# Kernel optimization log

Measured on AMD Instinct MI355X. Metric: run time of the kernel, lower is better.

## Reference

```python
import jax, jax.numpy as jnp
import numpy as np
import math

H = 12  # num_heads
LOGIT_SCALE_MAX = math.log(1.0 / 0.01)  # ~4.60517


def setup_inputs() -> dict:
    key = jax.random.key(0)
    ks = jax.random.split(key, 4)
    L, N, C = 1024, 8, 768
    scale = (C // H) ** -0.5
    return {
        "x": jax.random.normal(ks[0], (L, N, C), jnp.float32),
        "in_proj_weight": jax.random.normal(ks[1], (3 * C, C), jnp.float32) * scale,
        "in_proj_bias": jnp.zeros((3 * C,), jnp.float32),
        "logit_scale": jnp.full((H, 1, 1), jnp.log(10.0), jnp.float32),
        "head_scale": jnp.ones((H, 1, 1), jnp.float32),
        "out_w": jax.random.normal(ks[2], (C, C), jnp.float32) * scale,
        "out_b": jnp.zeros((C,), jnp.float32),
    }


def _normalize(t, eps=1e-12):
    # torch F.normalize: x / max(||x||, eps)
    n = jnp.linalg.norm(t, axis=-1, keepdims=True)
    return t / jnp.maximum(n, eps)


def reference(x, in_proj_weight, in_proj_bias, logit_scale, head_scale, out_w, out_b):
    L, N, C = x.shape
    D = C // H
    qkv = x @ in_proj_weight.T + in_proj_bias  # (L, N, 3C)
    q, k, v = jnp.split(qkv, 3, axis=-1)

    def to_heads(t):  # (L, N, C) -> (N, H, L, D); matches view(L, N*H, D).transpose(0,1)
        return t.reshape(L, N, H, D).transpose(1, 2, 0, 3)

    q, k, v = to_heads(q), to_heads(k), to_heads(v)
    # scaled-cosine attention: cosine sim * clamped-exp learnable logit scale
    attn = jnp.einsum('nhld,nhmd->nhlm', _normalize(q), _normalize(k))  # (N,H,L,L)
    ls = jnp.exp(jnp.minimum(logit_scale, LOGIT_SCALE_MAX))  # (H,1,1)
    attn = attn * ls[None]
    attn = jax.nn.softmax(attn, axis=-1)
    o = jnp.einsum('nhlm,nhmd->nhld', attn, v)  # (N,H,L,D)
    o = o * head_scale[None]  # per-head scale
    o = o.transpose(2, 0, 1, 3).reshape(L, N, C)  # back to (L, N, C)
    return o @ out_w.T + out_b
```

## Files before the change

kernel.cpp:

```cpp
#include <hip/hip_runtime.h>
#include <stdint.h>
#include <math.h>

typedef unsigned short u16;
typedef _Float16 f16;
typedef __attribute__((ext_vector_type(4))) float f32x4;
typedef __attribute__((ext_vector_type(8))) f16 h8;
typedef __attribute__((ext_vector_type(4))) f16 h4;
typedef __attribute__((ext_vector_type(2))) f16 h2;
typedef __attribute__((ext_vector_type(2))) __fp16 fp16x2;
typedef __attribute__((ext_vector_type(4))) unsigned int u32x4;
typedef __attribute__((ext_vector_type(4))) unsigned short u16x4;
typedef __attribute__((ext_vector_type(8))) unsigned short u16x8;

typedef const __attribute__((address_space(1))) u16 gas_u16;
typedef __attribute__((address_space(3))) u16 las_u16;

#define MFMA32(a,b,c) __builtin_amdgcn_mfma_f32_16x16x32_f16((a),(b),(c),0,0,0)
#define MFMA16(a,b,c) __builtin_amdgcn_mfma_f32_16x16x16f16((a),(b),(c),0,0,0)

__device__ __forceinline__ float h2f(u16 h){ f16 x; __builtin_memcpy(&x,&h,2); return (float)x; }
__device__ __forceinline__ u16 f2h(float f){ f16 x = (f16)f; u16 u; __builtin_memcpy(&u,&x,2); return u; }

__device__ __forceinline__ float fast_exp2(float x){
#if __has_builtin(__builtin_amdgcn_exp2f)
  return __builtin_amdgcn_exp2f(x);
#else
  return exp2f(x);
#endif
}

__device__ __forceinline__ h2 pkrtz(float a, float b){
  fp16x2 t = __builtin_amdgcn_cvt_pkrtz(a, b);
  h2 r; __builtin_memcpy(&r, &t, 4);
  return r;
}

#define NA4 1572864
#define NB4 442368
#define NC4 147456
__global__ __launch_bounds__(256) void cvt3_kernel(
    const float* __restrict__ a, u16* __restrict__ da,
    const float* __restrict__ b, u16* __restrict__ db,
    const float* __restrict__ c, u16* __restrict__ dc)
{
  int i = blockIdx.x*256 + threadIdx.x;
  const float* s; u16* d; int off;
  if (i < NA4)            { s = a; d = da; off = i; }
  else if (i < NA4+NB4)   { s = b; d = db; off = i - NA4; }
  else if (i < NA4+NB4+NC4){ s = c; d = dc; off = i - NA4 - NB4; }
  else return;
  f32x4 v = ((const f32x4*)s)[off];
  u16x4 o;
  o[0]=f2h(v[0]); o[1]=f2h(v[1]); o[2]=f2h(v[2]); o[3]=f2h(v[3]);
  ((u16x4*)d)[off] = o;
}

__global__ __launch_bounds__(256) void gemm_kernel(
    const u16* __restrict__ A, const u16* __restrict__ B, const float* __restrict__ bias,
    int mode, u16* __restrict__ qh, u16* __restrict__ kh, u16* __restrict__ vh,
    float* __restrict__ outp, const float* __restrict__ lsb)
{
  __shared__ u16 lA[2][128*64];
  __shared__ u16 lB[2][128*64];
  const int tid = threadIdx.x;
  const int lane = tid & 63;
  const int w = tid >> 6, wr = w >> 1, wc = w & 1;
  const int lo = lane & 15, hi = lane >> 4;

  const int bx = blockIdx.x, by = blockIdx.y;

  f32x4 zero = {0.f,0.f,0.f,0.f};
  f32x4 acc[4][4];
#pragma unroll
  for (int a=0;a<4;a++)
#pragma unroll
    for (int b=0;b<4;b++) acc[a][b] = zero;
  const u16* Ag = A + (size_t)bx*128*768;
  const u16* Bg = B + (size_t)by*128*768;
  const int srow = tid >> 3;
  const int scol = (((tid & 7) ^ (srow & 7)) * 8);

#define STAGE(buf, kt) do { \
    _Pragma("unroll") \
    for (int j=0;j<4;j++) { \
      __builtin_amdgcn_global_load_lds((gas_u16*)(Ag + (size_t)(j*32+srow)*768 + (kt) + scol), (las_u16*)(&lA[buf][j*2048 + tid*8]), 16, 0, 0); \
      __builtin_amdgcn_global_load_lds((gas_u16*)(Bg + (size_t)(j*32+srow)*768 + (kt) + scol), (las_u16*)(&lB[buf][j*2048 + tid*8]), 16, 0, 0); \
    } \
  } while(0)

  STAGE(0, 0);
#pragma unroll
  for (int t = 0; t < 12; ++t) {
    const int cur = t & 1;
    if (t < 11) {
      STAGE(cur^1, (t+1)*64);
      asm volatile("s_waitcnt vmcnt(8)" ::: "memory");
    } else {
      asm volatile("s_waitcnt vmcnt(0)" ::: "memory");
    }
    __builtin_amdgcn_sched_barrier(0);
    __builtin_amdgcn_s_barrier();
#pragma unroll
    for (int kk=0;kk<2;kk++) {
      h8 af[4], bfr[4];
#pragma unroll
      for (int mf=0; mf<4; mf++) {
        int r = wr*64 + mf*16 + lo;
        af[mf]  = *(const h8*)(&lA[cur][r*64 + (((hi + 4*kk) ^ (lo & 7)) * 8)]);
      }
#pragma unroll
      for (int nf=0; nf<4; nf++) {
        int r = wc*64 + nf*16 + lo;
        bfr[nf] = *(const h8*)(&lB[cur][r*64 + (((hi + 4*kk) ^ (lo & 7)) * 8)]);
      }
#pragma unroll
      for (int mf=0; mf<4; mf++)
#pragma unroll
        for (int nf=0; nf<4; nf++)
          acc[mf][nf] = MFMA32(af[mf], bfr[nf], acc[mf][nf]);
    }
    asm volatile("s_waitcnt lgkmcnt(0)" ::: "memory");
    __builtin_amdgcn_sched_barrier(0);
    __builtin_amdgcn_s_barrier();
  }
#undef STAGE

  const int r0 = bx*128 + wr*64;
  const int j0 = by*128 + wc*64;
  if (mode == 0) {
    const int p = (j0 >= 1536) ? 2 : ((j0 >= 768) ? 1 : 0);
    const int c0 = j0 - p*768;
    const int hh = c0 >> 6;
    u16* dst = (p==0) ? qh : ((p==1) ? kh : vh);
    float bi[4];
#pragma unroll
    for (int nf=0;nf<4;nf++) bi[nf] = bias[j0 + nf*16 + lo];
    float qsc = 1.0f;
    if (p == 0) qsc = __expf(fminf(lsb[hh], 4.6051701859880913680f)) * 1.4426950408889634f;
    const bool dnorm = (p != 2);
#pragma unroll
    for (int mf=0; mf<4; mf++)
#pragma unroll
      for (int i=0;i<4;i++) {
        int r = r0 + mf*16 + 4*hi + i;
        int n = r & 7, l = r >> 3;
        float v[4]; float ss = 0.f;
#pragma unroll
        for (int nf=0;nf<4;nf++){ v[nf] = acc[mf][nf][i] + bi[nf]; ss += v[nf]*v[nf]; }
        float sc = 1.0f;
        if (dnorm) {
          ss += __shfl_xor(ss, 1);
          ss += __shfl_xor(ss, 2);
          ss += __shfl_xor(ss, 4);
          ss += __shfl_xor(ss, 8);
          sc = qsc / fmaxf(sqrtf(ss), 1e-12f);
        }
        size_t base = (((size_t)n*12 + hh)*1024 + l)*64;
#pragma unroll
        for (int nf=0;nf<4;nf++)
          dst[base + nf*16 + lo] = f2h(v[nf]*sc);
      }
  } else {
#pragma unroll
    for (int nf=0; nf<4; nf++) {
      int j = j0 + nf*16 + lo;
      float bi = bias[j];
#pragma unroll
      for (int mf=0; mf<4; mf++)
#pragma unroll
        for (int i=0;i<4;i++) {
          int r = r0 + mf*16 + 4*hi + i;
          outp[(size_t)r*768 + j] = acc[mf][nf][i] + bi;
        }
    }
  }
}

__global__ __launch_bounds__(256) void transpose_kernel(const u16* __restrict__ vh, u16* __restrict__ vt){
  __shared__ u16 tile[64*72];
  const int nh = blockIdx.y, lt = blockIdx.x, tid = threadIdx.x;
  const int r = tid >> 2, c0 = (tid & 3) * 16;
  const u16* src = vh + (size_t)nh*65536 + (size_t)(lt*64 + r)*64 + c0;
  u32x4 a = *(const u32x4*)src, b = *(const u32x4*)(src + 8);
  *(u32x4*)(tile + r*72 + c0)     = a;
  *(u32x4*)(tile + r*72 + c0 + 8) = b;
  __syncthreads();
  u16x8 o0, o1;
#pragma unroll
  for (int s=0;s<8;s++){ o0[s] = tile[(c0+s)*72 + r]; o1[s] = tile[(c0+8+s)*72 + r]; }
  u16* dst = vt + (size_t)nh*65536 + (size_t)r*1024 + lt*64 + c0;
  *(u16x8*)dst       = o0;
  *(u16x8*)(dst + 8) = o1;
}

__global__ __launch_bounds__(256) void flash_kernel(
    const u16* __restrict__ qh, const u16* __restrict__ kh, const u16* __restrict__ vt,
    u16* __restrict__ obuf, const float* __restrict__ hsv, const float* __restrict__ lsp)
{
  __shared__ u16 lK[2*64*72];
  __shared__ u16 lVT[2*64*72];
  const int lin = blockIdx.y*8 + blockIdx.x;
  const int xcd = lin & 7, g = lin >> 3;
  const int nh = xcd + 8*(g >> 3);
  const int qt = g & 7;
  const int h = nh % 12, n = nh / 12;
  const u16* Qp = qh + (size_t)nh*65536;
  const u16* Kp = kh + (size_t)nh*65536;
  const u16* Vp = vt + (size_t)nh*65536;
  const int tid = threadIdx.x, lane = tid & 63, w = tid >> 6;
  const int lo = lane & 15, hi = lane >> 4;

  h8 qa0, qa1, qb0, qb1;
  {
    const u16* qrow = Qp + (size_t)(qt*128 + w*32 + lo)*64 + hi*8;
    qa0 = *(const h8*)qrow;          qa1 = *(const h8*)(qrow + 32);
    qb0 = *(const h8*)(qrow + 1024); qb1 = *(const h8*)(qrow + 1024 + 32);
  }
  const f32x4 zero = {0.f,0.f,0.f,0.f};
  f32x4 oA[4] = {zero,zero,zero,zero};
  f32x4 oB[4] = {zero,zero,zero,zero};
  f32x4 lA4 = zero, lB4 = zero;
  const h4 ones = {(f16)1.f,(f16)1.f,(f16)1.f,(f16)1.f};

  float OFF;
  {
    float b = __expf(fminf(lsp[h], 4.6051701859880913680f)) * 1.4426950408889634f;
    OFF = fmaxf(b - 15.5f, 0.f);
  }

  const int sr = tid >> 2;
  const int sc = (tid & 3) * 16;
  u32x4 ka, kb, va, vb;
  ka = *(const u32x4*)(Kp + (size_t)sr*64 + sc);
  kb = *(const u32x4*)(Kp + (size_t)sr*64 + sc + 8);
  va = *(const u32x4*)(Vp + (size_t)sr*1024 + sc);
  vb = *(const u32x4*)(Vp + (size_t)sr*1024 + sc + 8);
  *(u32x4*)(lK  + sr*72 + sc)     = ka;
  *(u32x4*)(lK  + sr*72 + sc + 8) = kb;
  *(u32x4*)(lVT + sr*72 + sc)     = va;
  *(u32x4*)(lVT + sr*72 + sc + 8) = vb;
  __syncthreads();

  for (int t = 0; t < 16; ++t) {
    const u16* cK = lK  + (t&1)*4608;
    const u16* cV = lVT + (t&1)*4608;
    u16* nK = lK  + ((t&1)^1)*4608;
    u16* nV = lVT + ((t&1)^1)*4608;
    if (t < 15) {
      ka = *(const u32x4*)(Kp + (size_t)(t+1)*4096 + (size_t)sr*64 + sc);
      kb = *(const u32x4*)(Kp + (size_t)(t+1)*4096 + (size_t)sr*64 + sc + 8);
      va = *(const u32x4*)(Vp + (size_t)sr*1024 + (t+1)*64 + sc);
      vb = *(const u32x4*)(Vp + (size_t)sr*1024 + (t+1)*64 + sc + 8);
    }
    f32x4 sa[4], sb[4];
#pragma unroll
    for (int kf=0; kf<4; kf++) {
      const u16* krow = cK + (kf*16 + lo)*72 + hi*8;
      h8 k0 = *(const h8*)krow;
      h8 k1 = *(const h8*)(krow + 32);
      sa[kf] = MFMA32(k1, qa1, MFMA32(k0, qa0, zero));
      sb[kf] = MFMA32(k1, qb1, MFMA32(k0, qb0, zero));
    }
    if (OFF != 0.f) {
#pragma unroll
      for (int kf=0;kf<4;kf++)
#pragma unroll
        for (int i=0;i<4;i++) { sa[kf][i] -= OFF; sb[kf][i] -= OFF; }
    }
    h4 pa[4], pb[4];
#pragma unroll
    for (int kf=0;kf<4;kf++) {
      h2 a01 = pkrtz(fast_exp2(sa[kf][0]), fast_exp2(sa[kf][1]));
      h2 a23 = pkrtz(fast_exp2(sa[kf][2]), fast_exp2(sa[kf][3]));
      pa[kf] = __builtin_shufflevector(a01, a23, 0, 1, 2, 3);
      h2 b01 = pkrtz(fast_exp2(sb[kf][0]), fast_exp2(sb[kf][1]));
      h2 b23 = pkrtz(fast_exp2(sb[kf][2]), fast_exp2(sb[kf][3]));
      pb[kf] = __builtin_shufflevector(b01, b23, 0, 1, 2, 3);
    }
#pragma unroll
    for (int kf=0;kf<4;kf++) {
      lA4 = MFMA16(ones, pa[kf], lA4);
      lB4 = MFMA16(ones, pb[kf], lB4);
    }
#pragma unroll
    for (int db=0; db<4; db++) {
#pragma unroll
      for (int kf=0; kf<4; kf++) {
        h4 vf = *(const h4*)(cV + (db*16 + lo)*72 + kf*16 + hi*4);
        oA[db] = MFMA16(vf, pa[kf], oA[db]);
        oB[db] = MFMA16(vf, pb[kf], oB[db]);
      }
    }
    if (t < 15) {
      *(u32x4*)(nK + sr*72 + sc)     = ka;
      *(u32x4*)(nK + sr*72 + sc + 8) = kb;
      *(u32x4*)(nV + sr*72 + sc)     = va;
      *(u32x4*)(nV + sr*72 + sc + 8) = vb;
    }
    __syncthreads();
  }
  float hsc = hsv[h];
  float invA = hsc / lA4[0];
  float invB = hsc / lB4[0];
  int l0 = qt*128 + w*32 + lo;
  u16* dA = obuf + ((size_t)l0*8 + n)*768 + h*64;
  u16* dB = obuf + ((size_t)(l0+16)*8 + n)*768 + h*64;
#pragma unroll
  for (int db=0; db<4; db++) {
    u16x4 pk0, pk1;
#pragma unroll
    for (int i=0;i<4;i++) { pk0[i] = f2h(oA[db][i]*invA); pk1[i] = f2h(oB[db][i]*invB); }
    *(u16x4*)(dA + db*16 + hi*4) = pk0;
    *(u16x4*)(dB + db*16 + hi*4) = pk1;
  }
}

extern "C" void kernel_launch(void* const* d_in, const int* in_sizes, int n_in,
                              void* d_out, int out_size, void* d_ws, size_t ws_size,
                              hipStream_t stream)
{
  (void)in_sizes; (void)n_in; (void)out_size; (void)ws_size;
  const float* x  = (const float*)d_in[0];
  const float* w1 = (const float*)d_in[1];
  const float* b1 = (const float*)d_in[2];
  const float* ls = (const float*)d_in[3];
  const float* hs = (const float*)d_in[4];
  const float* w2 = (const float*)d_in[5];
  const float* b2 = (const float*)d_in[6];
  float* out = (float*)d_out;

  u16* x_bf  = (u16*)d_ws;
  u16* w1_bf = x_bf  + 6291456;
  u16* w2_bf = w1_bf + 1769472;
  u16* qh    = w2_bf + 589824;
  u16* kh    = qh    + 6291456;
  u16* vh    = kh    + 6291456;
  u16* vt    = vh    + 6291456;
  u16* ob    = x_bf;

  cvt3_kernel<<<8448, 256, 0, stream>>>(x, x_bf, w1, w1_bf, w2, w2_bf);
  gemm_kernel<<<dim3(64,18), 256, 0, stream>>>(x_bf, w1_bf, b1, 0, qh, kh, vh, nullptr, ls);
  transpose_kernel<<<dim3(16,96), 256, 0, stream>>>(vh, vt);
  flash_kernel<<<dim3(8,96), 256, 0, stream>>>(qh, kh, vt, ob, hs, ls);
  gemm_kernel<<<dim3(64,6), 256, 0, stream>>>(ob, w2_bf, b2, 1, nullptr, nullptr, nullptr, out, ls);
}
```

Baseline: 130.6 us.

## Halve flash query tile, single-buffer swizzled LDS, raise occupancy

The flash kernel now handles 64 query rows per block instead of 128 and launches twice as many blocks. K and V tiles move from padded double-buffered shared memory to single-buffered 64x64 tiles with an XOR swizzle, which cuts LDS use and lets V fragments load as wider 8-element reads. Launch bounds request 6 waves per SIMD to raise occupancy. In exchange, K/V tiles are fetched twice as often per query row, and the loop needs two barriers per iteration since prefetch can no longer overlap with a second buffer.

```diff
diff --git a/kernel.cpp b/kernel.cpp
--- a/kernel.cpp
+++ b/kernel.cpp
@@ -9,6 +9,7 @@
 typedef __attribute__((ext_vector_type(4))) f16 h4;
 typedef __attribute__((ext_vector_type(2))) f16 h2;
 typedef __attribute__((ext_vector_type(2))) __fp16 fp16x2;
+typedef __attribute__((ext_vector_type(2))) unsigned int u32x2;
 typedef __attribute__((ext_vector_type(4))) unsigned int u32x4;
 typedef __attribute__((ext_vector_type(4))) unsigned short u16x4;
 typedef __attribute__((ext_vector_type(8))) unsigned short u16x8;
@@ -194,33 +195,33 @@
   *(u16x8*)(dst + 8) = o1;
 }
 
-__global__ __launch_bounds__(256) void flash_kernel(
+__global__ __launch_bounds__(256, 6) void flash_kernel(
     const u16* __restrict__ qh, const u16* __restrict__ kh, const u16* __restrict__ vt,
     u16* __restrict__ obuf, const float* __restrict__ hsv, const float* __restrict__ lsp)
 {
-  __shared__ u16 lK[2*64*72];
-  __shared__ u16 lVT[2*64*72];
-  const int lin = blockIdx.y*8 + blockIdx.x;
+  __shared__ u16 lK[64*64];
+  __shared__ u16 lVT[64*64];
+  const int lin = blockIdx.y*16 + blockIdx.x;
   const int xcd = lin & 7, g = lin >> 3;
-  const int nh = xcd + 8*(g >> 3);
-  const int qt = g & 7;
+  const int nh = xcd + 8*(g >> 4);
+  const int qt = g & 15;
   const int h = nh % 12, n = nh / 12;
   const u16* Qp = qh + (size_t)nh*65536;
   const u16* Kp = kh + (size_t)nh*65536;
   const u16* Vp = vt + (size_t)nh*65536;
   const int tid = threadIdx.x, lane = tid & 63, w = tid >> 6;
   const int lo = lane & 15, hi = lane >> 4;
-
-  h8 qa0, qa1, qb0, qb1;
+  const int e = lo & 7;
+
+  h8 qa0, qa1;
   {
-    const u16* qrow = Qp + (size_t)(qt*128 + w*32 + lo)*64 + hi*8;
-    qa0 = *(const h8*)qrow;          qa1 = *(const h8*)(qrow + 32);
-    qb0 = *(const h8*)(qrow + 1024); qb1 = *(const h8*)(qrow + 1024 + 32);
+    const u16* qrow = Qp + (size_t)(qt*64 + w*16 + lo)*64 + hi*8;
+    qa0 = *(const h8*)qrow;
+    qa1 = *(const h8*)(qrow + 32);
   }
   const f32x4 zero = {0.f,0.f,0.f,0.f};
   f32x4 oA[4] = {zero,zero,zero,zero};
-  f32x4 oB[4] = {zero,zero,zero,zero};
-  f32x4 lA4 = zero, lB4 = zero;
+  f32x4 lA4 = zero;
   const h4 ones = {(f16)1.f,(f16)1.f,(f16)1.f,(f16)1.f};
 
   float OFF;
@@ -230,89 +231,82 @@
   }
 
   const int sr = tid >> 2;
-  const int sc = (tid & 3) * 16;
+  const int c4 = tid & 3;
+  const int sx1 = sr & 7;
+  const int sx2 = (sr & 7) << 1;
+
   u32x4 ka, kb, va, vb;
-  ka = *(const u32x4*)(Kp + (size_t)sr*64 + sc);
-  kb = *(const u32x4*)(Kp + (size_t)sr*64 + sc + 8);
-  va = *(const u32x4*)(Vp + (size_t)sr*1024 + sc);
-  vb = *(const u32x4*)(Vp + (size_t)sr*1024 + sc + 8);
-  *(u32x4*)(lK  + sr*72 + sc)     = ka;
-  *(u32x4*)(lK  + sr*72 + sc + 8) = kb;
-  *(u32x4*)(lVT + sr*72 + sc)     = va;
-  *(u32x4*)(lVT + sr*72 + sc + 8) = vb;
-  __syncthreads();
+  ka = *(const u32x4*)(Kp + (size_t)sr*64 + c4*16);
+  kb = *(const u32x4*)(Kp + (size_t)sr*64 + c4*16 + 8);
+  va = *(const u32x4*)(Vp + (size_t)sr*1024 + c4*16);
+  vb = *(const u32x4*)(Vp + (size_t)sr*1024 + c4*16 + 8);
 
   for (int t = 0; t < 16; ++t) {
-    const u16* cK = lK  + (t&1)*4608;
-    const u16* cV = lVT + (t&1)*4608;
-    u16* nK = lK  + ((t&1)^1)*4608;
-    u16* nV = lVT + ((t&1)^1)*4608;
+    {
+      u16* kr = lK + sr*64;
+      *(u32x4*)(kr + (((2*c4)   ^ sx1) << 3)) = ka;
+      *(u32x4*)(kr + (((2*c4+1) ^ sx1) << 3)) = kb;
+      u16* vr = lVT + sr*64;
+      *(u32x2*)(vr + (((( 0|c4) ^ sx2) << 2))) = (u32x2){va[0], va[1]};
+      *(u32x2*)(vr + (((( 4|c4) ^ sx2) << 2))) = (u32x2){va[2], va[3]};
+      *(u32x2*)(vr + (((( 8|c4) ^ sx2) << 2))) = (u32x2){vb[0], vb[1]};
+      *(u32x2*)(vr + ((((12|c4) ^ sx2) << 2))) = (u32x2){vb[2], vb[3]};
+    }
+    asm volatile("s_waitcnt lgkmcnt(0)" ::: "memory");
+    __builtin_amdgcn_sched_barrier(0);
+    __builtin_amdgcn_s_barrier();
     if (t < 15) {
-      ka = *(const u32x4*)(Kp + (size_t)(t+1)*4096 + (size_t)sr*64 + sc);
-      kb = *(const u32x4*)(Kp + (size_t)(t+1)*4096 + (size_t)sr*64 + sc + 8);
-      va = *(const u32x4*)(Vp + (size_t)sr*1024 + (t+1)*64 + sc);
-      vb = *(const u32x4*)(Vp + (size_t)sr*1024 + (t+1)*64 + sc + 8);
-    }
-    f32x4 sa[4], sb[4];
+      ka = *(const u32x4*)(Kp + (size_t)(t+1)*4096 + (size_t)sr*64 + c4*16);
+      kb = *(const u32x4*)(Kp + (size_t)(t+1)*4096 + (size_t)sr*64 + c4*16 + 8);
+      va = *(const u32x4*)(Vp + (size_t)sr*1024 + (t+1)*64 + c4*16);
+      vb = *(const u32x4*)(Vp + (size_t)sr*1024 + (t+1)*64 + c4*16 + 8);
+    }
+    f32x4 sa[4];
 #pragma unroll
     for (int kf=0; kf<4; kf++) {
-      const u16* krow = cK + (kf*16 + lo)*72 + hi*8;
-      h8 k0 = *(const h8*)krow;
-      h8 k1 = *(const h8*)(krow + 32);
+      const u16* krow = lK + (kf*16 + lo)*64;
+      h8 k0 = *(const h8*)(krow + (((hi  ) ^ e) << 3));
+      h8 k1 = *(const h8*)(krow + (((hi+4) ^ e) << 3));
       sa[kf] = MFMA32(k1, qa1, MFMA32(k0, qa0, zero));
-      sb[kf] = MFMA32(k1, qb1, MFMA32(k0, qb0, zero));
     }
     if (OFF != 0.f) {
 #pragma unroll
       for (int kf=0;kf<4;kf++)
 #pragma unroll
-        for (int i=0;i<4;i++) { sa[kf][i] -= OFF; sb[kf][i] -= OFF; }
-    }
-    h4 pa[4], pb[4];
+        for (int i=0;i<4;i++) sa[kf][i] -= OFF;
+    }
+    h4 pa[4];
 #pragma unroll
     for (int kf=0;kf<4;kf++) {
       h2 a01 = pkrtz(fast_exp2(sa[kf][0]), fast_exp2(sa[kf][1]));
       h2 a23 = pkrtz(fast_exp2(sa[kf][2]), fast_exp2(sa[kf][3]));
       pa[kf] = __builtin_shufflevector(a01, a23, 0, 1, 2, 3);
-      h2 b01 = pkrtz(fast_exp2(sb[kf][0]), fast_exp2(sb[kf][1]));
-      h2 b23 = pkrtz(fast_exp2(sb[kf][2]), fast_exp2(sb[kf][3]));
-      pb[kf] = __builtin_shufflevector(b01, b23, 0, 1, 2, 3);
-    }
-#pragma unroll
-    for (int kf=0;kf<4;kf++) {
-      lA4 = MFMA16(ones, pa[kf], lA4);
-      lB4 = MFMA16(ones, pb[kf], lB4);
-    }
+    }
+#pragma unroll
+    for (int kf=0;kf<4;kf++) lA4 = MFMA16(ones, pa[kf], lA4);
 #pragma unroll
     for (int db=0; db<4; db++) {
-#pragma unroll
-      for (int kf=0; kf<4; kf++) {
-        h4 vf = *(const h4*)(cV + (db*16 + lo)*72 + kf*16 + hi*4);
-        oA[db] = MFMA16(vf, pa[kf], oA[db]);
-        oB[db] = MFMA16(vf, pb[kf], oB[db]);
-      }
-    }
-    if (t < 15) {
-      *(u32x4*)(nK + sr*72 + sc)     = ka;
-      *(u32x4*)(nK + sr*72 + sc + 8) = kb;
-      *(u32x4*)(nV + sr*72 + sc)     = va;
-      *(u32x4*)(nV + sr*72 + sc + 8) = vb;
-    }
-    __syncthreads();
-  }
-  float hsc = hsv[h];
-  float invA = hsc / lA4[0];
-  float invB = hsc / lB4[0];
-  int l0 = qt*128 + w*32 + lo;
-  u16* dA = obuf + ((size_t)l0*8 + n)*768 + h*64;
-  u16* dB = obuf + ((size_t)(l0+16)*8 + n)*768 + h*64;
+      const u16* vrow = lVT + (db*16 + lo)*64;
+      h8 v01 = *(const h8*)(vrow + ((((2*hi  ) ^ e) << 3)));
+      h8 v23 = *(const h8*)(vrow + ((((2*hi+1) ^ e) << 3)));
+      oA[db] = MFMA16(__builtin_shufflevector(v01, v01, 0,1,2,3), pa[0], oA[db]);
+      oA[db] = MFMA16(__builtin_shufflevector(v01, v01, 4,5,6,7), pa[1], oA[db]);
+      oA[db] = MFMA16(__builtin_shufflevector(v23, v23, 0,1,2,3), pa[2], oA[db]);
+      oA[db] = MFMA16(__builtin_shufflevector(v23, v23, 4,5,6,7), pa[3], oA[db]);
+    }
+    asm volatile("s_waitcnt lgkmcnt(0)" ::: "memory");
+    __builtin_amdgcn_sched_barrier(0);
+    __builtin_amdgcn_s_barrier();
+  }
+  float inv = hsv[h] / lA4[0];
+  int l = qt*64 + w*16 + lo;
+  u16* dst = obuf + ((size_t)l*8 + n)*768 + h*64;
 #pragma unroll
   for (int db=0; db<4; db++) {
-    u16x4 pk0, pk1;
-#pragma unroll
-    for (int i=0;i<4;i++) { pk0[i] = f2h(oA[db][i]*invA); pk1[i] = f2h(oB[db][i]*invB); }
-    *(u16x4*)(dA + db*16 + hi*4) = pk0;
-    *(u16x4*)(dB + db*16 + hi*4) = pk1;
+    u16x4 pk;
+#pragma unroll
+    for (int i=0;i<4;i++) pk[i] = f2h(oA[db][i] * inv);
+    *(u16x4*)(dst + db*16 + hi*4) = pk;
   }
 }
 
@@ -342,6 +336,6 @@
   cvt3_kernel<<<8448, 256, 0, stream>>>(x, x_bf, w1, w1_bf, w2, w2_bf);
   gemm_kernel<<<dim3(64,18), 256, 0, stream>>>(x_bf, w1_bf, b1, 0, qh, kh, vh, nullptr, ls);
   transpose_kernel<<<dim3(16,96), 256, 0, stream>>>(vh, vt);
-  flash_kernel<<<dim3(8,96), 256, 0, stream>>>(qh, kh, vt, ob, hs, ls);
+  flash_kernel<<<dim3(16,96), 256, 0, stream>>>(qh, kh, vt, ob, hs, ls);
   gemm_kernel<<<dim3(64,6), 256, 0, stream>>>(ob, w2_bf, b2, 1, nullptr, nullptr, nullptr, out, ls);
 }
```

Result: faster. 126.0 us (-3.5%).
